# Optimization experiments

Hardware: AMD Instinct MI355X
Metric: run time of the kernel (lower is better)

## Reference

```python
import jax, jax.numpy as jnp
import numpy as np

B, IN, H = 4096, 2048, 2048


def setup_inputs() -> dict:
    key = jax.random.key(0)
    ks = jax.random.split(key, 20)
    s_in = 1.0 / np.sqrt(IN)
    s_h = 1.0 / np.sqrt(H)
    inp = {
        "x": jax.random.normal(ks[0], (B, IN), jnp.float32),
        "h": jax.random.normal(ks[1], (B, H), jnp.float32),
        "c": jax.random.normal(ks[2], (B, H), jnp.float32),
    }
    names_in = [("Wii", "bii"), ("Wif", "bif"), ("Wig", "big"), ("Wio", "bio")]
    names_h = [("Whi", "bhi"), ("Whf", "bhf"), ("Whg", "bhg"), ("Who", "bho")]
    k = 3
    for wn, bn in names_in:
        inp[wn] = jax.random.normal(ks[k], (H, IN), jnp.float32) * s_in
        inp[bn] = jax.random.normal(ks[k + 1], (H,), jnp.float32) * s_in
        k += 2
    for wn, bn in names_h:
        inp[wn] = jax.random.normal(ks[k], (H, H), jnp.float32) * s_h
        inp[bn] = jax.random.normal(ks[k + 1], (H,), jnp.float32) * s_h
        k += 2
    return inp


def reference(x, h, c, Wii, bii, Whi, bhi, Wif, bif, Whf, bhf,
              Wig, big, Whg, bhg, Wio, bio, Who, bho):
    # Fuse the 4 input-projections and 4 hidden-projections into two GEMMs
    # (same math as 8 separate nn.Linear calls).
    Wx = jnp.concatenate([Wii, Wif, Wig, Wio], axis=0)   # [4H, IN]
    Wh = jnp.concatenate([Whi, Whf, Whg, Who], axis=0)   # [4H, H]
    bx = jnp.concatenate([bii, bif, big, bio])            # [4H]
    bh = jnp.concatenate([bhi, bhf, bhg, bho])            # [4H]
    gates = x @ Wx.T + h @ Wh.T + bx + bh                 # [B, 4H]
    ii, ff, gg, oo = jnp.split(gates, 4, axis=-1)
    i = jax.nn.sigmoid(ii)
    f = jax.nn.sigmoid(ff)
    g = jnp.tanh(gg)
    o = jax.nn.sigmoid(oo)
    c_new = f * c + i * g
    h_new = o * jnp.tanh(c_new)
    return jnp.stack([h_new, c_new])  # [2, B, H]
```

## Files before the change

### kernel.cpp

```cpp
#include <hip/hip_runtime.h>
#include <stdint.h>

typedef __attribute__((ext_vector_type(4))) float f32x4;
typedef __attribute__((ext_vector_type(8))) short bf16x8;

#define MFMA_BF16 __builtin_amdgcn_mfma_f32_16x16x32_bf16

__device__ __forceinline__ unsigned short f2bf(float f) {
  union { float f; uint32_t u; } a; a.f = f;
  uint32_t u = a.u;
  uint32_t r = (u + 0x7FFFu + ((u >> 16) & 1u)) >> 16;
  return (unsigned short)r;
}

__global__ void pack_a_kernel(const float4* __restrict__ x, const float4* __restrict__ hh,
                              ushort4* __restrict__ A) {
  const int total = 4096 * 1024;
  for (int q = blockIdx.x * blockDim.x + threadIdx.x; q < total; q += gridDim.x * blockDim.x) {
    int row = q >> 10, cq = q & 1023;
    float4 v = (cq < 512) ? x[row * 512 + cq] : hh[row * 512 + (cq - 512)];
    ushort4 o; o.x = f2bf(v.x); o.y = f2bf(v.y); o.z = f2bf(v.z); o.w = f2bf(v.w);
    A[q] = o;
  }
}

__global__ void pack_w_kernel(const float* __restrict__ Wii, const float* __restrict__ Wif,
                              const float* __restrict__ Wig, const float* __restrict__ Wio,
                              const float* __restrict__ Whi, const float* __restrict__ Whf,
                              const float* __restrict__ Whg, const float* __restrict__ Who,
                              ushort4* __restrict__ Wp) {
  const int total = 8192 * 1024;
  for (int q = blockIdx.x * blockDim.x + threadIdx.x; q < total; q += gridDim.x * blockDim.x) {
    int p = q >> 10, kq = q & 1023;
    int r = p & 255;
    int g = ((r >> 7) << 1) | ((r >> 4) & 1);
    int H = ((p >> 8) << 6) | (((r >> 5) & 3) << 4) | (r & 15);
    const float* src;
    if (kq < 512) src = (g == 0) ? Wii : (g == 1) ? Wif : (g == 2) ? Wig : Wio;
    else          src = (g == 0) ? Whi : (g == 1) ? Whf : (g == 2) ? Whg : Who;
    const float4 v = *(const float4*)&src[(size_t)H * 2048 + ((kq & 511) << 2)];
    ushort4 o; o.x = f2bf(v.x); o.y = f2bf(v.y); o.z = f2bf(v.z); o.w = f2bf(v.w);
    Wp[q] = o;
  }
}

#define GLD(srcp, dstE)                                                         \
  __builtin_amdgcn_global_load_lds(                                             \
      (const __attribute__((address_space(1))) void*)(srcp),                    \
      (__attribute__((address_space(3))) void*)(&smem[dstE]), 16, 0, 0)

#define STAGE(t_)                                                               \
  {                                                                             \
    const int rr_ = ((t_) & 3) << 14;                                           \
    const size_t kO_ = (size_t)(t_) * 32;                                       \
    GLD(aS + kO_, rr_ + dA);                                                    \
    GLD(aS + 524288 + kO_, rr_ + dA + 4096);                                    \
    GLD(bS + kO_, rr_ + dB);                                                    \
    GLD(bS + 524288 + kO_, rr_ + dB + 4096);                                    \
  }

__global__ __launch_bounds__(512, 2)
void lstm_gemm_kernel(const ushort* __restrict__ A, const ushort* __restrict__ Wp,
                      const float* __restrict__ c,
                      const float* __restrict__ bii, const float* __restrict__ bif_,
                      const float* __restrict__ big_, const float* __restrict__ bio_,
                      const float* __restrict__ bhi, const float* __restrict__ bhf,
                      const float* __restrict__ bhg, const float* __restrict__ bho,
                      float* __restrict__ out) {
  __shared__ ushort smem[65536];
  const int tid = threadIdx.x;
  const int lane = tid & 63, w = tid >> 6;
  const int wm = w >> 2, wn = w & 3;

  const int bid = blockIdx.x;
  const int xcd = bid & 7, qq = bid >> 3;
  const int bn = (xcd << 2) | (qq >> 4);
  const int bm = qq & 15;

  const int laneRow = lane & 15, lane16 = lane >> 4;
  const int chunkSwz = lane16 ^ ((laneRow >> 1) & 3);
  const int rdCommon = (laneRow >> 1) * 64 + (laneRow & 1) * 32 + chunkSwz * 8;
  const int aRB = wm * 2048 + rdCommon;
  const int bRB = 8192 + wn * 1024 + rdCommon;

  const int lrow = 2 * (lane >> 3) + ((lane >> 2) & 1);
  const int schunk = (lane & 3) ^ ((lane >> 3) & 3);
  const ushort* aS = A + (size_t)(bm * 256 + 16 * w + lrow) * 4096 + schunk * 8;
  const ushort* bS = Wp + (size_t)(bn * 256 + 16 * w + lrow) * 4096 + schunk * 8;
  const int dA = w * 512;
  const int dB = 8192 + w * 512;

  f32x4 acc[8][4];
#pragma unroll
  for (int i = 0; i < 8; i++)
#pragma unroll
    for (int j = 0; j < 4; j++) acc[i][j] = (f32x4){0.f, 0.f, 0.f, 0.f};

  STAGE(0); STAGE(1); STAGE(2);
  asm volatile("s_waitcnt vmcnt(8)" ::: "memory");
  __builtin_amdgcn_s_barrier();
  __builtin_amdgcn_sched_barrier(0);

#pragma unroll 1
  for (int T = 0; T < 128; ++T) {
    const int ring = (T & 3) << 14;
    if (T < 125) STAGE(T + 3);

    bf16x8 bf[4], af0[4], af1[4];
#pragma unroll
    for (int ni = 0; ni < 4; ++ni)
      bf[ni] = *(const bf16x8*)&smem[ring + bRB + (ni >> 1) * 4096 + (ni & 1) * 512];
#pragma unroll
    for (int m = 0; m < 4; ++m)
      af0[m] = *(const bf16x8*)&smem[ring + aRB + m * 512];
    __builtin_amdgcn_s_setprio(1);
#pragma unroll
    for (int m = 0; m < 4; ++m)
#pragma unroll
      for (int ni = 0; ni < 4; ++ni)
        acc[m][ni] = MFMA_BF16(af0[m], bf[ni], acc[m][ni], 0, 0, 0);
    __builtin_amdgcn_s_setprio(0);
#pragma unroll
    for (int m = 0; m < 4; ++m)
      af1[m] = *(const bf16x8*)&smem[ring + aRB + 4096 + m * 512];
    __builtin_amdgcn_s_setprio(1);
#pragma unroll
    for (int m = 0; m < 4; ++m)
#pragma unroll
      for (int ni = 0; ni < 4; ++ni)
        acc[4 + m][ni] = MFMA_BF16(af1[m], bf[ni], acc[4 + m][ni], 0, 0, 0);
    __builtin_amdgcn_s_setprio(0);

    if (T < 125)       asm volatile("s_waitcnt vmcnt(8)" ::: "memory");
    else if (T == 125) asm volatile("s_waitcnt vmcnt(4)" ::: "memory");
    else if (T == 126) asm volatile("s_waitcnt vmcnt(0)" ::: "memory");
    if (T < 127) {
      __builtin_amdgcn_s_barrier();
      __builtin_amdgcn_sched_barrier(0);
    }
  }

  const int hcol = bn * 64 + wn * 16 + laneRow;
  const float bI = bii[hcol] + bhi[hcol];
  const float bF = bif_[hcol] + bhf[hcol];
  const float bG = big_[hcol] + bhg[hcol];
  const float bO = bio_[hcol] + bho[hcol];
#pragma unroll
  for (int mi = 0; mi < 8; ++mi) {
    const int rowBase = bm * 256 + (mi >> 2) * 128 + wm * 64 + (mi & 3) * 16 + lane16 * 4;
#pragma unroll
    for (int rr = 0; rr < 4; ++rr) {
      const int row = rowBase + rr;
      const float ii = acc[mi][0][rr] + bI;
      const float ff = acc[mi][1][rr] + bF;
      const float gg = acc[mi][2][rr] + bG;
      const float oo = acc[mi][3][rr] + bO;
      const float iv = 1.f / (1.f + __expf(-ii));
      const float fv = 1.f / (1.f + __expf(-ff));
      const float gv = tanhf(gg);
      const float ov = 1.f / (1.f + __expf(-oo));
      const float cv = c[(size_t)row * 2048 + hcol];
      const float cn = fv * cv + iv * gv;
      const float hn = ov * tanhf(cn);
      out[(size_t)row * 2048 + hcol] = hn;
      out[(size_t)8388608 + (size_t)row * 2048 + hcol] = cn;
    }
  }
}

extern "C" void kernel_launch(void* const* d_in, const int* in_sizes, int n_in,
                              void* d_out, int out_size, void* d_ws, size_t ws_size,
                              hipStream_t stream) {
  const float* x = (const float*)d_in[0];
  const float* h = (const float*)d_in[1];
  const float* c = (const float*)d_in[2];
  const float* Wii = (const float*)d_in[3];  const float* bii = (const float*)d_in[4];
  const float* Wif = (const float*)d_in[5];  const float* bif_ = (const float*)d_in[6];
  const float* Wig = (const float*)d_in[7];  const float* big_ = (const float*)d_in[8];
  const float* Wio = (const float*)d_in[9];  const float* bio_ = (const float*)d_in[10];
  const float* Whi = (const float*)d_in[11]; const float* bhi = (const float*)d_in[12];
  const float* Whf = (const float*)d_in[13]; const float* bhf = (const float*)d_in[14];
  const float* Whg = (const float*)d_in[15]; const float* bhg = (const float*)d_in[16];
  const float* Who = (const float*)d_in[17]; const float* bho = (const float*)d_in[18];

  ushort* Abf = (ushort*)d_ws;
  ushort* Wpk = Abf + (size_t)4096 * 4096;
  float* out = (float*)d_out;

  pack_a_kernel<<<2048, 256, 0, stream>>>((const float4*)x, (const float4*)h, (ushort4*)Abf);
  pack_w_kernel<<<2048, 256, 0, stream>>>(Wii, Wif, Wig, Wio, Whi, Whf, Whg, Who, (ushort4*)Wpk);
  lstm_gemm_kernel<<<512, 512, 0, stream>>>(Abf, Wpk, c,
                                            bii, bif_, big_, bio_, bhi, bhf, bhg, bho, out);
}
```

Measured before the change: 332.0 us.

## Double-buffer LDS fragment reads and unroll the K loop by four

Restructures the GEMM main loop so each step loads the next tile's A/B fragments from LDS into a second register set while MFMAs run on the current set. The loop is unrolled by the 4-deep ring, so ring offsets become compile-time constants, and the wait-count logic is rewritten to match. The intent is to hide LDS read latency behind the matrix instructions and to drop per-iteration index arithmetic. The cost is 12 extra bf16x8 fragment registers per lane, on top of 128 accumulator registers under __launch_bounds__(512, 2). That adds register pressure and a possible risk of spills.

```diff
diff --git a/kernel.cpp b/kernel.cpp
--- a/kernel.cpp
+++ b/kernel.cpp
@@ -49,15 +49,35 @@
       (const __attribute__((address_space(1))) void*)(srcp),                    \
       (__attribute__((address_space(3))) void*)(&smem[dstE]), 16, 0, 0)
 
-#define STAGE(t_)                                                               \
+#define STAGE_R(t_, ringB_)                                                     \
   {                                                                             \
-    const int rr_ = ((t_) & 3) << 14;                                           \
     const size_t kO_ = (size_t)(t_) * 32;                                       \
-    GLD(aS + kO_, rr_ + dA);                                                    \
-    GLD(aS + 524288 + kO_, rr_ + dA + 4096);                                    \
-    GLD(bS + kO_, rr_ + dB);                                                    \
-    GLD(bS + 524288 + kO_, rr_ + dB + 4096);                                    \
-  }
+    GLD(aS + kO_, (ringB_) + dA);                                               \
+    GLD(aS + 524288 + kO_, (ringB_) + dA + 4096);                               \
+    GLD(bS + kO_, (ringB_) + dB);                                               \
+    GLD(bS + 524288 + kO_, (ringB_) + dB + 4096);                               \
+  }
+
+#define PREF(RN_, AF_, BF_)                                                     \
+  {                                                                             \
+    _Pragma("unroll") for (int n = 0; n < 4; ++n)                               \
+      BF_[n] = *(const bf16x8*)&smem[(RN_) + bRB + (n >> 1) * 4096 + (n & 1) * 512]; \
+    _Pragma("unroll") for (int m = 0; m < 4; ++m)                               \
+      AF_[m] = *(const bf16x8*)&smem[(RN_) + aRB + m * 512];                    \
+    _Pragma("unroll") for (int m = 0; m < 4; ++m)                               \
+      AF_[4 + m] = *(const bf16x8*)&smem[(RN_) + aRB + 4096 + m * 512];         \
+  }
+
+#define COMP(AF_, BF_)                                                          \
+  {                                                                             \
+    __builtin_amdgcn_s_setprio(1);                                              \
+    _Pragma("unroll") for (int m = 0; m < 8; ++m)                               \
+      _Pragma("unroll") for (int n = 0; n < 4; ++n)                             \
+        acc[m][n] = MFMA_BF16(AF_[m], BF_[n], acc[m][n], 0, 0, 0);              \
+    __builtin_amdgcn_s_setprio(0);                                              \
+  }
+
+#define SB0 __builtin_amdgcn_sched_barrier(0)
 
 __global__ __launch_bounds__(512, 2)
 void lstm_gemm_kernel(const ushort* __restrict__ A, const ushort* __restrict__ Wp,
@@ -96,49 +116,57 @@
 #pragma unroll
     for (int j = 0; j < 4; j++) acc[i][j] = (f32x4){0.f, 0.f, 0.f, 0.f};
 
-  STAGE(0); STAGE(1); STAGE(2);
-  asm volatile("s_waitcnt vmcnt(8)" ::: "memory");
+  STAGE_R(0, 0); STAGE_R(1, 16384); STAGE_R(2, 32768);
+  asm volatile("s_waitcnt vmcnt(4)" ::: "memory");
   __builtin_amdgcn_s_barrier();
-  __builtin_amdgcn_sched_barrier(0);
+  SB0;
+
+  bf16x8 afA[8], bfA[4], afB[8], bfB[4];
+  PREF(0, afA, bfA);
 
 #pragma unroll 1
-  for (int T = 0; T < 128; ++T) {
-    const int ring = (T & 3) << 14;
-    if (T < 125) STAGE(T + 3);
-
-    bf16x8 bf[4], af0[4], af1[4];
-#pragma unroll
-    for (int ni = 0; ni < 4; ++ni)
-      bf[ni] = *(const bf16x8*)&smem[ring + bRB + (ni >> 1) * 4096 + (ni & 1) * 512];
-#pragma unroll
-    for (int m = 0; m < 4; ++m)
-      af0[m] = *(const bf16x8*)&smem[ring + aRB + m * 512];
-    __builtin_amdgcn_s_setprio(1);
-#pragma unroll
-    for (int m = 0; m < 4; ++m)
-#pragma unroll
-      for (int ni = 0; ni < 4; ++ni)
-        acc[m][ni] = MFMA_BF16(af0[m], bf[ni], acc[m][ni], 0, 0, 0);
-    __builtin_amdgcn_s_setprio(0);
-#pragma unroll
-    for (int m = 0; m < 4; ++m)
-      af1[m] = *(const bf16x8*)&smem[ring + aRB + 4096 + m * 512];
-    __builtin_amdgcn_s_setprio(1);
-#pragma unroll
-    for (int m = 0; m < 4; ++m)
-#pragma unroll
-      for (int ni = 0; ni < 4; ++ni)
-        acc[4 + m][ni] = MFMA_BF16(af1[m], bf[ni], acc[4 + m][ni], 0, 0, 0);
-    __builtin_amdgcn_s_setprio(0);
-
-    if (T < 125)       asm volatile("s_waitcnt vmcnt(8)" ::: "memory");
-    else if (T == 125) asm volatile("s_waitcnt vmcnt(4)" ::: "memory");
-    else if (T == 126) asm volatile("s_waitcnt vmcnt(0)" ::: "memory");
-    if (T < 127) {
-      __builtin_amdgcn_s_barrier();
-      __builtin_amdgcn_sched_barrier(0);
-    }
-  }
+  for (int TT = 0; TT < 124; TT += 4) {
+    STAGE_R(TT + 3, 49152);
+    PREF(16384, afB, bfB);
+    SB0;
+    COMP(afA, bfA);
+    asm volatile("s_waitcnt vmcnt(4)" ::: "memory");
+    __builtin_amdgcn_s_barrier(); SB0;
+    STAGE_R(TT + 4, 0);
+    PREF(32768, afA, bfA);
+    SB0;
+    COMP(afB, bfB);
+    asm volatile("s_waitcnt vmcnt(4)" ::: "memory");
+    __builtin_amdgcn_s_barrier(); SB0;
+    STAGE_R(TT + 5, 16384);
+    PREF(49152, afB, bfB);
+    SB0;
+    COMP(afA, bfA);
+    asm volatile("s_waitcnt vmcnt(4)" ::: "memory");
+    __builtin_amdgcn_s_barrier(); SB0;
+    STAGE_R(TT + 6, 32768);
+    PREF(0, afA, bfA);
+    SB0;
+    COMP(afB, bfB);
+    asm volatile("s_waitcnt vmcnt(4)" ::: "memory");
+    __builtin_amdgcn_s_barrier(); SB0;
+  }
+
+  STAGE_R(127, 49152);
+  PREF(16384, afB, bfB);
+  SB0;
+  COMP(afA, bfA);
+  asm volatile("s_waitcnt vmcnt(4)" ::: "memory");
+  __builtin_amdgcn_s_barrier(); SB0;
+  PREF(32768, afA, bfA);
+  SB0;
+  COMP(afB, bfB);
+  asm volatile("s_waitcnt vmcnt(0)" ::: "memory");
+  __builtin_amdgcn_s_barrier(); SB0;
+  PREF(49152, afB, bfB);
+  SB0;
+  COMP(afA, bfA);
+  COMP(afB, bfB);
 
   const int hcol = bn * 64 + wn * 16 + laneRow;
   const float bI = bii[hcol] + bhi[hcol];
```

Measured after the change: 334.2 us. Within noise of the previous version (+0.7%).
